# Kernel tuning notes

Measured on AMD Instinct MI355X. Metric: run time of the kernel, lower is better.

## Reference

```python
import jax, jax.numpy as jnp
import numpy as np

T, P, N = 16, 250000, 20  # steps, n_params, n_inputs


def setup_inputs() -> dict:
    key = jax.random.key(0)
    ks = jax.random.split(key, 7)
    x_all = jax.random.normal(ks[0], (T, P, N), dtype=jnp.float32)          # [steps, n_params, n_inputs]
    grad = jax.random.normal(ks[1], (T,), dtype=jnp.float32) * 0.1           # one learner-grad scalar per step (grad[i])
    WF = jax.random.normal(ks[2], (N + 2, 1), dtype=jnp.float32) * 0.05      # forget-gate weights
    WI = jax.random.normal(ks[3], (N + 2, 1), dtype=jnp.float32) * 0.05      # input-gate weights
    cI = jax.random.normal(ks[4], (P, 1), dtype=jnp.float32) * 0.05          # initial cell state (flat learner params)
    bF = jax.random.uniform(ks[5], (1, 1), minval=8.0, maxval=10.0, dtype=jnp.float32)
    bI = jax.random.uniform(ks[6], (1, 1), minval=-5.0, maxval=-4.0, dtype=jnp.float32)
    return {"x_all": x_all, "grad": grad, "WF": WF, "WI": WI, "cI": cI, "bF": bF, "bI": bI}


def reference(x_all, grad, WF, WI, cI, bF, bI):
    n_params = x_all.shape[1]
    f0 = jnp.zeros((n_params, 1), dtype=x_all.dtype)
    i0 = jnp.zeros((n_params, 1), dtype=x_all.dtype)

    def step(carry, inp):
        f_prev, i_prev, c_prev = carry
        x_t, g_t = inp  # x_t: [P, N], g_t: scalar
        f_next = jnp.concatenate([x_t, c_prev, f_prev], axis=1) @ WF + bF  # [P, 1]
        i_next = jnp.concatenate([x_t, c_prev, i_prev], axis=1) @ WI + bI  # [P, 1]
        c_next = jax.nn.sigmoid(f_next) * c_prev - jax.nn.sigmoid(i_next) * g_t
        return (f_next, i_next, c_next), None

    (f_T, i_T, c_T), _ = jax.lax.scan(step, (f0, i0, cI), (x_all, grad))
    # original returns (cx, [f, i, cx])
    return (c_T, f_T, i_T)
```

## Files before the change

### kernel.cpp

```cpp
#include <hip/hip_runtime.h>


#define T_STEPS 16
#define N_IN 20

__global__ __launch_bounds__(256) void metalstm_kernel(
    const float* __restrict__ x_all,
    const float* __restrict__ grad,
    const float* __restrict__ WF,
    const float* __restrict__ WI,
    const float* __restrict__ cI,
    const float* __restrict__ bF,
    const float* __restrict__ bI,
    float* __restrict__ out,
    int P)
{
    const int p = blockIdx.x * blockDim.x + threadIdx.x;
    if (p >= P) return;

    float wF[22], wI[22];
#pragma unroll
    for (int k = 0; k < 22; ++k) { wF[k] = WF[k]; wI[k] = WI[k]; }
    const float biasF = bF[0];
    const float biasI = bI[0];

    float f = 0.0f;
    float ii = 0.0f;
    float c = cI[p];

#pragma unroll 2
    for (int t = 0; t < T_STEPS; ++t) {
        const float4* xp = reinterpret_cast<const float4*>(
            x_all + ((long)t * P + p) * N_IN);
        const float4 v0 = xp[0];
        const float4 v1 = xp[1];
        const float4 v2 = xp[2];
        const float4 v3 = xp[3];
        const float4 v4 = xp[4];
        const float g_t = grad[t];

        float dF = biasF, dI = biasI;
#define ACC(val, k) dF = fmaf((val), wF[(k)], dF); dI = fmaf((val), wI[(k)], dI);
        ACC(v0.x, 0)  ACC(v0.y, 1)  ACC(v0.z, 2)  ACC(v0.w, 3)
        ACC(v1.x, 4)  ACC(v1.y, 5)  ACC(v1.z, 6)  ACC(v1.w, 7)
        ACC(v2.x, 8)  ACC(v2.y, 9)  ACC(v2.z, 10) ACC(v2.w, 11)
        ACC(v3.x, 12) ACC(v3.y, 13) ACC(v3.z, 14) ACC(v3.w, 15)
        ACC(v4.x, 16) ACC(v4.y, 17) ACC(v4.z, 18) ACC(v4.w, 19)
#undef ACC

        const float fn = fmaf(c, wF[20], fmaf(f, wF[21], dF));
        const float in_ = fmaf(c, wI[20], fmaf(ii, wI[21], dI));
        const float sf = 1.0f / (1.0f + expf(-fn));
        const float si = 1.0f / (1.0f + expf(-in_));
        c = sf * c - si * g_t;
        f = fn;
        ii = in_;
    }

    out[p]         = c;
    out[P + p]     = f;
    out[2 * P + p] = ii;
}

extern "C" void kernel_launch(void* const* d_in, const int* in_sizes, int n_in,
                              void* d_out, int out_size, void* d_ws, size_t ws_size,
                              hipStream_t stream) {
    const float* x_all = (const float*)d_in[0];
    const float* grad  = (const float*)d_in[1];
    const float* WF    = (const float*)d_in[2];
    const float* WI    = (const float*)d_in[3];
    const float* cI    = (const float*)d_in[4];
    const float* bF    = (const float*)d_in[5];
    const float* bI    = (const float*)d_in[6];
    float* out = (float*)d_out;

    const int P = in_sizes[4];
    const int block = 256;
    const int grid = (P + block - 1) / block;
    metalstm_kernel<<<grid, block, 0, stream>>>(x_all, grad, WF, WI, cI, bF, bI, out, P);
}
```

Measured before the change: 62.83 us.

## Stage x rows through LDS with coalesced loads and register prefetch

```diff
diff --git a/kernel.cpp b/kernel.cpp
--- a/kernel.cpp
+++ b/kernel.cpp
@@ -1,10 +1,11 @@
 #include <hip/hip_runtime.h>
 
 
-#define T_STEPS 16
+#define BLOCK 256
 #define N_IN 20
+#define ROW_F4 5
 
-__global__ __launch_bounds__(256) void metalstm_kernel(
+__global__ __launch_bounds__(BLOCK) void metalstm_kernel(
     const float* __restrict__ x_all,
     const float* __restrict__ grad,
     const float* __restrict__ WF,
@@ -13,10 +14,15 @@
     const float* __restrict__ bF,
     const float* __restrict__ bI,
     float* __restrict__ out,
-    int P)
+    int P, int T)
 {
-    const int p = blockIdx.x * blockDim.x + threadIdx.x;
-    if (p >= P) return;
+    __shared__ __align__(16) float4 xs4[BLOCK * ROW_F4];
+
+    const int tid = threadIdx.x;
+    const int pbase = blockIdx.x * BLOCK;
+    const int p = pbase + tid;
+    const bool valid = (p < P);
+    const int pc = valid ? p : (P - 1);
 
     float wF[22], wI[22];
 #pragma unroll
@@ -26,40 +32,67 @@
 
     float f = 0.0f;
     float ii = 0.0f;
-    float c = cI[p];
+    float c = cI[pc];
 
-#pragma unroll 2
-    for (int t = 0; t < T_STEPS; ++t) {
-        const float4* xp = reinterpret_cast<const float4*>(
-            x_all + ((long)t * P + p) * N_IN);
-        const float4 v0 = xp[0];
-        const float4 v1 = xp[1];
-        const float4 v2 = xp[2];
-        const float4 v3 = xp[3];
-        const float4 v4 = xp[4];
+    const float4* __restrict__ x4 = reinterpret_cast<const float4*>(x_all);
+
+    float4 pr0, pr1, pr2, pr3, pr4;
+    {
+        const long base4 = (long)P * 0 * ROW_F4 + (long)pbase * ROW_F4;
+        const long end4  = ((long)P * 0 + P) * ROW_F4;
+#define LOADK(k, dst) { long idx = base4 + tid + (k) * BLOCK; \
+                        if (idx >= end4) idx = end4 - 1; \
+                        dst = x4[idx]; }
+        LOADK(0, pr0) LOADK(1, pr1) LOADK(2, pr2) LOADK(3, pr3) LOADK(4, pr4)
+    }
+
+    for (int t = 0; t < T; ++t) {
+        __syncthreads();
+
+#define STOREK(k, src) { const int fidx = tid + (k) * BLOCK; \
+                         const int row = fidx / ROW_F4; \
+                         const int sl  = fidx - row * ROW_F4; \
+                         int slr = sl + row % ROW_F4; if (slr >= ROW_F4) slr -= ROW_F4; \
+                         xs4[row * ROW_F4 + slr] = src; }
+        STOREK(0, pr0) STOREK(1, pr1) STOREK(2, pr2) STOREK(3, pr3) STOREK(4, pr4)
+#undef STOREK
+        __syncthreads();
+
+        if (t + 1 < T) {
+            const long base4 = ((long)(t + 1) * P + pbase) * ROW_F4;
+            const long end4  = ((long)(t + 1) * P + P) * ROW_F4;
+            LOADK(0, pr0) LOADK(1, pr1) LOADK(2, pr2) LOADK(3, pr3) LOADK(4, pr4)
+        }
+
         const float g_t = grad[t];
 
         float dF = biasF, dI = biasI;
-#define ACC(val, k) dF = fmaf((val), wF[(k)], dF); dI = fmaf((val), wI[(k)], dI);
-        ACC(v0.x, 0)  ACC(v0.y, 1)  ACC(v0.z, 2)  ACC(v0.w, 3)
-        ACC(v1.x, 4)  ACC(v1.y, 5)  ACC(v1.z, 6)  ACC(v1.w, 7)
-        ACC(v2.x, 8)  ACC(v2.y, 9)  ACC(v2.z, 10) ACC(v2.w, 11)
-        ACC(v3.x, 12) ACC(v3.y, 13) ACC(v3.z, 14) ACC(v3.w, 15)
-        ACC(v4.x, 16) ACC(v4.y, 17) ACC(v4.z, 18) ACC(v4.w, 19)
-#undef ACC
+        const int rbase = tid * ROW_F4;
+        const int rrot  = tid % ROW_F4;
+#define ACC4(jj) { int slr = (jj) + rrot; if (slr >= ROW_F4) slr -= ROW_F4; \
+                   const float4 v = xs4[rbase + slr]; \
+                   dF = fmaf(v.x, wF[4*(jj)+0], dF); dI = fmaf(v.x, wI[4*(jj)+0], dI); \
+                   dF = fmaf(v.y, wF[4*(jj)+1], dF); dI = fmaf(v.y, wI[4*(jj)+1], dI); \
+                   dF = fmaf(v.z, wF[4*(jj)+2], dF); dI = fmaf(v.z, wI[4*(jj)+2], dI); \
+                   dF = fmaf(v.w, wF[4*(jj)+3], dF); dI = fmaf(v.w, wI[4*(jj)+3], dI); }
+        ACC4(0) ACC4(1) ACC4(2) ACC4(3) ACC4(4)
+#undef ACC4
 
-        const float fn = fmaf(c, wF[20], fmaf(f, wF[21], dF));
+        const float fn  = fmaf(c, wF[20], fmaf(f,  wF[21], dF));
         const float in_ = fmaf(c, wI[20], fmaf(ii, wI[21], dI));
-        const float sf = 1.0f / (1.0f + expf(-fn));
-        const float si = 1.0f / (1.0f + expf(-in_));
+        const float sf = 1.0f / (1.0f + __expf(-fn));
+        const float si = 1.0f / (1.0f + __expf(-in_));
         c = sf * c - si * g_t;
         f = fn;
         ii = in_;
     }
+#undef LOADK
 
-    out[p]         = c;
-    out[P + p]     = f;
-    out[2 * P + p] = ii;
+    if (valid) {
+        out[p]         = c;
+        out[P + p]     = f;
+        out[2 * P + p] = ii;
+    }
 }
 
 extern "C" void kernel_launch(void* const* d_in, const int* in_sizes, int n_in,
@@ -75,7 +108,7 @@
     float* out = (float*)d_out;
 
     const int P = in_sizes[4];
-    const int block = 256;
-    const int grid = (P + block - 1) / block;
-    metalstm_kernel<<<grid, block, 0, stream>>>(x_all, grad, WF, WI, cI, bF, bI, out, P);
+    const int T = in_sizes[1];
+    const int grid = (P + BLOCK - 1) / BLOCK;
+    metalstm_kernel<<<grid, BLOCK, 0, stream>>>(x_all, grad, WF, WI, cI, bF, bI, out, P, T);
 }
```

New measurement: 55.77 us. -11.2%, faster.
